# Performance work log

Measured on AMD Instinct MI355X. Metric: run time of the kernel, lower is better.

The kernel has to match this reference:

```python
import jax, jax.numpy as jnp
import numpy as np

NUM_HEADS = 16
DK = 64
DV = 64
MASK_FILL = -10000000000.0


def setup_inputs() -> dict:
    key = jax.random.key(0)
    kq, kk, kv, km = jax.random.split(key, 4)
    B, L, D = 2, 2048, NUM_HEADS * DK
    Q = jax.random.normal(kq, (B, L, D), dtype=jnp.float32)
    K = jax.random.normal(kk, (B, L, D), dtype=jnp.float32)
    V = jax.random.normal(kv, (B, L, NUM_HEADS * DV), dtype=jnp.float32)
    mask = jax.random.randint(km, (B, L, L), 0, 2).astype(jnp.bool_)
    return {"Q": Q, "K": K, "V": V, "mask": mask}


def reference(Q, K, V, mask):
    B, Lq, _ = Q.shape
    Lk = K.shape[1]
    # split heads: [B, H, L, d]
    q = Q.reshape(B, Lq, NUM_HEADS, DK).transpose(0, 2, 1, 3)
    k = K.reshape(B, Lk, NUM_HEADS, DK).transpose(0, 2, 1, 3)
    v = V.reshape(B, Lk, NUM_HEADS, DV).transpose(0, 2, 1, 3)
    # scores [B, H, Lq, Lk]; NOTE: original masks BEFORE scaling by 1/sqrt(dk)
    scores = jnp.einsum("bhqd,bhkd->bhqk", q, k)
    scores = jnp.where(mask[:, None, :, :], MASK_FILL, scores)
    scores = scores / jnp.sqrt(jnp.asarray(DK, dtype=scores.dtype))
    attn = jax.nn.softmax(scores, axis=-1)
    out = jnp.einsum("bhqk,bhkd->bhqd", attn, v)  # [B, H, Lq, dv]
    # concat heads back: [B, Lq, H*dv]
    return out.transpose(0, 2, 1, 3).reshape(B, Lq, NUM_HEADS * DV)
```

## Files before the change

kernel.cpp:

```cpp
#include <hip/hip_runtime.h>
#include <hip/hip_bf16.h>

#define NH 16
#define DH 64
#define LL 2048
#define DM 1024
#define SCALE2 0.1803368801111204f
#define GUARD_HI 60.0f
#define NT2 (LL / 128)

typedef __attribute__((ext_vector_type(4))) float f32x4;
typedef __attribute__((ext_vector_type(8))) short bf16x8;
typedef __attribute__((ext_vector_type(4))) short bf16x4;

__device__ __forceinline__ unsigned pk2(float lo, float hi) {
    __hip_bfloat162 h = __float22bfloat162_rn(make_float2(lo, hi));
    union { __hip_bfloat162 h; unsigned u; } c; c.h = h; return c.u;
}
__device__ __forceinline__ bf16x8 cvt8(float4 a, float4 b) {
    union { bf16x8 v; unsigned u[4]; } r;
    r.u[0] = pk2(a.x, a.y); r.u[1] = pk2(a.z, a.w);
    r.u[2] = pk2(b.x, b.y); r.u[3] = pk2(b.z, b.w);
    return r.v;
}
__device__ __forceinline__ float exp2_fast(float x) {
    float y;
    asm("v_exp_f32 %0, %1" : "=v"(y) : "v"(x));
    return y;
}
__device__ __forceinline__ float keepf(float p, unsigned nw, int idx) {
    int k = (int)(nw << (31 - idx)) >> 31;
    unsigned pu = __builtin_bit_cast(unsigned, p) & (unsigned)k;
    return __builtin_bit_cast(float, pu);
}

__global__ __launch_bounds__(256) void pack_mask2(const void* __restrict__ mask,
                                                  unsigned* __restrict__ bits)
{
    const int tid = threadIdx.x;
    const int lane = tid & 63;
    const int* mw = (const int*)mask;
    unsigned long long bad = __ballot((unsigned)mw[lane] > 1u);
    const bool is_int = (bad == 0ULL);

    const int wid = blockIdx.x * 256 + tid;
    const int g = wid & 3;
    const int t = (wid >> 2) & 15;
    const int q64 = wid >> 6;
    unsigned m = 0;
    if (is_int) {
        const int* p = (const int*)mask + (size_t)q64 * LL + t * 128 + 4 * g;
        #pragma unroll
        for (int sub = 0; sub < 2; ++sub)
            #pragma unroll
            for (int ki = 0; ki < 4; ++ki) {
                int4 v = *(const int4*)(p + sub * 64 + ki * 16);
                int base = sub * 16 + ki * 4;
                m |= (v.x ? 1u : 0u) << base;
                m |= (v.y ? 1u : 0u) << (base + 1);
                m |= (v.z ? 1u : 0u) << (base + 2);
                m |= (v.w ? 1u : 0u) << (base + 3);
            }
    } else {
        const unsigned char* pb = (const unsigned char*)mask
                                + (size_t)q64 * LL + t * 128 + 4 * g;
        #pragma unroll
        for (int sub = 0; sub < 2; ++sub)
            #pragma unroll
            for (int ki = 0; ki < 4; ++ki) {
                unsigned v = *(const unsigned*)(pb + sub * 64 + ki * 16);
                int base = sub * 16 + ki * 4;
                m |= (v & 1u) << base;
                m |= ((v >> 8) & 1u) << (base + 1);
                m |= ((v >> 16) & 1u) << (base + 2);
                m |= ((v >> 24) & 1u) << (base + 3);
            }
    }
    bits[wid] = ~m;
}

__global__ __launch_bounds__(256) void prep_k(const float* __restrict__ K,
                                              short* __restrict__ Kb)
{
    const int kt = blockIdx.x, h = blockIdx.y, b = blockIdx.z;
    const int tid = threadIdx.x;
    const int key = tid >> 2;
    const int c8 = (tid & 3) * 2;
    const float* src = K + ((size_t)b * LL + kt * 64 + key) * DM + h * DH + c8 * 8;
    float4 a = *(const float4*)(src);
    float4 bb = *(const float4*)(src + 4);
    float4 c = *(const float4*)(src + 8);
    float4 d = *(const float4*)(src + 12);
    short* dst = Kb + (((size_t)(b * NH + h) * 32 + kt) << 12);
    *(bf16x8*)&dst[key * 64 + ((c8 ^ (key & 7)) << 3)] = cvt8(a, bb);
    *(bf16x8*)&dst[key * 64 + (((c8 + 1) ^ (key & 7)) << 3)] = cvt8(c, d);
}

__global__ __launch_bounds__(256) void prep_v(const float* __restrict__ V,
                                              short* __restrict__ Vb)
{
    const int kt = blockIdx.x, h = blockIdx.y, b = blockIdx.z;
    const int tid = threadIdx.x;
    const int kp = tid & 31;
    const int dv8 = tid >> 5;
    const float* s0 = V + ((size_t)b * LL + kt * 64 + 2 * kp) * DM + h * DH + dv8 * 8;
    float4 a0 = *(const float4*)(s0);
    float4 a1 = *(const float4*)(s0 + 4);
    float4 b0 = *(const float4*)(s0 + DM);
    float4 b1 = *(const float4*)(s0 + DM + 4);
    float av[8] = {a0.x, a0.y, a0.z, a0.w, a1.x, a1.y, a1.z, a1.w};
    float bv[8] = {b0.x, b0.y, b0.z, b0.w, b1.x, b1.y, b1.z, b1.w};
    short* dst = Vb + (((size_t)(b * NH + h) * 32 + kt) << 12);
    const int grp = ((kp >> 4) << 2) | ((kp >> 1) & 3);
    const int sub4 = (((kp >> 3) & 1) << 2) | ((kp & 1) << 1);
    #pragma unroll
    for (int j = 0; j < 8; ++j) {
        int dv = dv8 * 8 + j;
        int off = dv * 64 + ((grp ^ (dv & 7)) << 3) + sub4;
        *(unsigned*)&dst[off] = pk2(av[j], bv[j]);
    }
}

__global__ __launch_bounds__(512, 4) void mha_fwd2(
    const float* __restrict__ Q, const short* __restrict__ Kb,
    const short* __restrict__ Vb, const unsigned* __restrict__ mbits,
    float* __restrict__ out)
{
    const int bid = blockIdx.x;
    const int xcd = bid & 7;
    const int j = bid >> 3;
    const int pair = xcd * 4 + (j >> 4);
    const int qblk = j & 15;
    const int h = pair & 15;
    const int b = pair >> 4;

    const int tid = threadIdx.x;
    const int w = tid >> 6;
    const int lane = tid & 63;
    const int lq = lane & 15;
    const int g = lane >> 4;

    const int qbase = qblk * 128 + w * 16;

    __shared__ short Kt[2][2][4096];
    __shared__ short Vt[2][2][4096];

    const short* Ktile0 = Kb + ((size_t)(b * NH + h) << 17);
    const short* Vtile0 = Vb + ((size_t)(b * NH + h) << 17);
    const unsigned* Mp = mbits + ((size_t)b * LL + qbase + lq) * 64 + g;

    unsigned mnext = Mp[0];
    #pragma unroll
    for (int sub = 0; sub < 2; ++sub) {
        __builtin_amdgcn_global_load_lds(
            (const unsigned*)(Ktile0 + sub * 4096 + w * 512 + lane * 8),
            (unsigned*)&Kt[0][sub][w * 512], 16, 0, 0);
        __builtin_amdgcn_global_load_lds(
            (const unsigned*)(Vtile0 + sub * 4096 + w * 512 + lane * 8),
            (unsigned*)&Vt[0][sub][w * 512], 16, 0, 0);
    }

    bf16x8 qf[2];
    {
        const float* qrow = Q + ((size_t)b * LL + qbase + lq) * DM + h * DH;
        #pragma unroll
        for (int half = 0; half < 2; ++half) {
            const float* src = qrow + half * 32 + g * 8;
            float4 a = *(const float4*)(src);
            float4 c = *(const float4*)(src + 4);
            a.x *= SCALE2; a.y *= SCALE2; a.z *= SCALE2; a.w *= SCALE2;
            c.x *= SCALE2; c.y *= SCALE2; c.z *= SCALE2; c.w *= SCALE2;
            qf[half] = cvt8(a, c);
        }
    }

    f32x4 o[4];
    #pragma unroll
    for (int t = 0; t < 4; ++t) o[t] = (f32x4){0.f, 0.f, 0.f, 0.f};
    f32x4 l_acc = (f32x4){0.f, 0.f, 0.f, 0.f};
    float m_shift = 0.f;
    const bf16x4 ones = {(short)0x3F80, (short)0x3F80, (short)0x3F80, (short)0x3F80};

    asm volatile("s_waitcnt vmcnt(0)" ::: "memory");
    __builtin_amdgcn_s_barrier();

    #pragma unroll 2
    for (int t = 0; t < NT2; ++t) {
        const int cur = t & 1;
        const unsigned nword = mnext;
        if (t + 1 < NT2) {
            mnext = Mp[(t + 1) * 4];
            const short* kb = Ktile0 + (size_t)(t + 1) * 8192;
            const short* vb = Vtile0 + (size_t)(t + 1) * 8192;
            #pragma unroll
            for (int sub = 0; sub < 2; ++sub) {
                __builtin_amdgcn_global_load_lds(
                    (const unsigned*)(kb + sub * 4096 + w * 512 + lane * 8),
                    (unsigned*)&Kt[cur ^ 1][sub][w * 512], 16, 0, 0);
                __builtin_amdgcn_global_load_lds(
                    (const unsigned*)(vb + sub * 4096 + w * 512 + lane * 8),
                    (unsigned*)&Vt[cur ^ 1][sub][w * 512], 16, 0, 0);
            }
            asm volatile("s_waitcnt vmcnt(5)" ::: "memory");
        } else {
            asm volatile("s_waitcnt vmcnt(0)" ::: "memory");
        }
        __builtin_amdgcn_s_barrier();
        __builtin_amdgcn_sched_barrier(0);

        f32x4 sAB[2][4];
        __builtin_amdgcn_s_setprio(1);
        #pragma unroll
        for (int sub = 0; sub < 2; ++sub)
            #pragma unroll
            for (int ki = 0; ki < 4; ++ki) {
                const int row = ki * 16 + lq;
                bf16x8 k0 = *(const bf16x8*)
                    &Kt[cur][sub][row * 64 + ((g ^ (lq & 7)) << 3)];
                bf16x8 k1 = *(const bf16x8*)
                    &Kt[cur][sub][row * 64 + (((4 + g) ^ (lq & 7)) << 3)];
                f32x4 acc = (f32x4){0.f, 0.f, 0.f, 0.f};
                acc = __builtin_amdgcn_mfma_f32_16x16x32_bf16(k0, qf[0], acc, 0, 0, 0);
                acc = __builtin_amdgcn_mfma_f32_16x16x32_bf16(k1, qf[1], acc, 0, 0, 0);
                sAB[sub][ki] = acc;
            }
        __builtin_amdgcn_s_setprio(0);

        float mm[8];
        #pragma unroll
        for (int i = 0; i < 8; ++i) {
            f32x4 v = sAB[i >> 2][i & 3];
            mm[i] = fmaxf(fmaxf(v[0], v[1]), fmaxf(v[2], v[3]));
        }
        float mx = fmaxf(fmaxf(fmaxf(mm[0], mm[1]), fmaxf(mm[2], mm[3])),
                         fmaxf(fmaxf(mm[4], mm[5]), fmaxf(mm[6], mm[7])));
        if (__builtin_expect(m_shift != 0.0f, 0)) {
            #pragma unroll
            for (int i = 0; i < 8; ++i) sAB[i >> 2][i & 3] = sAB[i >> 2][i & 3] - m_shift;
            mx -= m_shift;
        }
        if (!__all(mx <= GUARD_HI)) {
            float tmax = fmaxf(mx, __shfl_xor(mx, 16, 64));
            tmax = fmaxf(tmax, __shfl_xor(tmax, 32, 64));
            float shift = tmax - 30.0f;
            m_shift += shift;
            float alpha = exp2_fast(-shift);
            #pragma unroll
            for (int q = 0; q < 4; ++q) {
                o[q][0] *= alpha; o[q][1] *= alpha;
                o[q][2] *= alpha; o[q][3] *= alpha;
            }
            l_acc[0] *= alpha; l_acc[1] *= alpha;
            l_acc[2] *= alpha; l_acc[3] *= alpha;
            #pragma unroll
            for (int i = 0; i < 8; ++i) sAB[i >> 2][i & 3] = sAB[i >> 2][i & 3] - shift;
        }

        #pragma unroll
        for (int sub = 0; sub < 2; ++sub) {
            union { bf16x4 v; unsigned u[2]; } pf[4];
            #pragma unroll
            for (int ki = 0; ki < 4; ++ki) {
                f32x4 sv = sAB[sub][ki];
                const int base = sub * 16 + ki * 4;
                float p0 = keepf(exp2_fast(sv[0]), nword, base + 0);
                float p1 = keepf(exp2_fast(sv[1]), nword, base + 1);
                float p2 = keepf(exp2_fast(sv[2]), nword, base + 2);
                float p3 = keepf(exp2_fast(sv[3]), nword, base + 3);
                pf[ki].u[0] = pk2(p0, p1);
                pf[ki].u[1] = pk2(p2, p3);
                l_acc = __builtin_amdgcn_mfma_f32_16x16x16bf16_1k(ones, pf[ki].v, l_acc, 0, 0, 0);
            }
            __builtin_amdgcn_s_setprio(1);
            #pragma unroll
            for (int P = 0; P < 2; ++P)
                #pragma unroll
                for (int q = 0; q < 4; ++q) {
                    const int row = 16 * q + lq;
                    bf16x8 v8 = *(const bf16x8*)
                        &Vt[cur][sub][row * 64 + ((((P << 2) + g) ^ (lq & 7)) << 3)];
                    bf16x4 vlo = {v8[0], v8[1], v8[2], v8[3]};
                    bf16x4 vhi = {v8[4], v8[5], v8[6], v8[7]};
                    o[q] = __builtin_amdgcn_mfma_f32_16x16x16bf16_1k(vlo, pf[2 * P].v, o[q], 0, 0, 0);
                    o[q] = __builtin_amdgcn_mfma_f32_16x16x16bf16_1k(vhi, pf[2 * P + 1].v, o[q], 0, 0, 0);
                }
            __builtin_amdgcn_s_setprio(0);
        }

        __builtin_amdgcn_sched_barrier(0);
        __builtin_amdgcn_s_barrier();
    }

    float inv = __builtin_amdgcn_rcpf(l_acc[0]);
    float* orow = out + ((size_t)b * LL + qbase + lq) * DM + h * DH;
    #pragma unroll
    for (int t = 0; t < 4; ++t) {
        float4 ov;
        ov.x = o[t][0] * inv; ov.y = o[t][1] * inv;
        ov.z = o[t][2] * inv; ov.w = o[t][3] * inv;
        *(float4*)(orow + 16 * t + 4 * g) = ov;
    }
}

extern "C" void kernel_launch(void* const* d_in, const int* in_sizes, int n_in,
                              void* d_out, int out_size, void* d_ws, size_t ws_size,
                              hipStream_t stream) {
    const float* Q = (const float*)d_in[0];
    const float* K = (const float*)d_in[1];
    const float* V = (const float*)d_in[2];
    const void* mask = d_in[3];
    float* out = (float*)d_out;

    unsigned* bits = (unsigned*)d_ws;
    const size_t MASK_B = (size_t)2 * LL * 64 * 4;
    const size_t KV_B = (size_t)2 * NH * 32 * 4096 * 2;
    short* Kb = (short*)((char*)d_ws + MASK_B);
    short* Vb = (short*)((char*)d_ws + MASK_B + KV_B);

    pack_mask2<<<dim3(2 * LL * 64 / 256), dim3(256), 0, stream>>>(mask, bits);
    prep_k<<<dim3(32, NH, 2), dim3(256), 0, stream>>>(K, Kb);
    prep_v<<<dim3(32, NH, 2), dim3(256), 0, stream>>>(V, Vb);
    mha_fwd2<<<dim3(512), dim3(512), 0, stream>>>(Q, Kb, Vb, bits, out);
}
```

Baseline: 80.69 us.

## Switch attention kernel to 32x32x16 MFMA with 32-query waves

```diff
diff --git a/kernel.cpp b/kernel.cpp
--- a/kernel.cpp
+++ b/kernel.cpp
@@ -10,8 +10,8 @@
 #define NT2 (LL / 128)
 
 typedef __attribute__((ext_vector_type(4))) float f32x4;
+typedef __attribute__((ext_vector_type(16))) float f32x16;
 typedef __attribute__((ext_vector_type(8))) short bf16x8;
-typedef __attribute__((ext_vector_type(4))) short bf16x4;
 
 __device__ __forceinline__ unsigned pk2(float lo, float hi) {
     __hip_bfloat162 h = __float22bfloat162_rn(make_float2(lo, hi));
@@ -34,7 +34,7 @@
     return __builtin_bit_cast(float, pu);
 }
 
-__global__ __launch_bounds__(256) void pack_mask2(const void* __restrict__ mask,
+__global__ __launch_bounds__(256) void pack_mask4(const void* __restrict__ mask,
                                                   unsigned* __restrict__ bits)
 {
     const int tid = threadIdx.x;
@@ -44,18 +44,20 @@
     const bool is_int = (bad == 0ULL);
 
     const int wid = blockIdx.x * 256 + tid;
-    const int g = wid & 3;
-    const int t = (wid >> 2) & 15;
-    const int q64 = wid >> 6;
+    const int kb = wid & 3;
+    const int q = (wid >> 2) & 2047;
+    const int t = (wid >> 13) & 15;
+    const int b = wid >> 17;
     unsigned m = 0;
     if (is_int) {
-        const int* p = (const int*)mask + (size_t)q64 * LL + t * 128 + 4 * g;
-        #pragma unroll
-        for (int sub = 0; sub < 2; ++sub)
-            #pragma unroll
-            for (int ki = 0; ki < 4; ++ki) {
-                int4 v = *(const int4*)(p + sub * 64 + ki * 16);
-                int base = sub * 16 + ki * 4;
+        const int* p = (const int*)mask + ((size_t)b * 2048 + q) * 2048
+                     + t * 128 + kb * 32;
+        #pragma unroll
+        for (int h = 0; h < 2; ++h)
+            #pragma unroll
+            for (int blk = 0; blk < 4; ++blk) {
+                int4 v = *(const int4*)(p + 8 * blk + 4 * h);
+                int base = 8 * blk + 4 * h;
                 m |= (v.x ? 1u : 0u) << base;
                 m |= (v.y ? 1u : 0u) << (base + 1);
                 m |= (v.z ? 1u : 0u) << (base + 2);
@@ -63,13 +65,13 @@
             }
     } else {
         const unsigned char* pb = (const unsigned char*)mask
-                                + (size_t)q64 * LL + t * 128 + 4 * g;
-        #pragma unroll
-        for (int sub = 0; sub < 2; ++sub)
-            #pragma unroll
-            for (int ki = 0; ki < 4; ++ki) {
-                unsigned v = *(const unsigned*)(pb + sub * 64 + ki * 16);
-                int base = sub * 16 + ki * 4;
+                                + ((size_t)b * 2048 + q) * 2048 + t * 128 + kb * 32;
+        #pragma unroll
+        for (int h = 0; h < 2; ++h)
+            #pragma unroll
+            for (int blk = 0; blk < 4; ++blk) {
+                unsigned v = *(const unsigned*)(pb + 8 * blk + 4 * h);
+                int base = 8 * blk + 4 * h;
                 m |= (v & 1u) << base;
                 m |= ((v >> 8) & 1u) << (base + 1);
                 m |= ((v >> 16) & 1u) << (base + 2);
@@ -111,17 +113,20 @@
     float av[8] = {a0.x, a0.y, a0.z, a0.w, a1.x, a1.y, a1.z, a1.w};
     float bv[8] = {b0.x, b0.y, b0.z, b0.w, b1.x, b1.y, b1.z, b1.w};
     short* dst = Vb + (((size_t)(b * NH + h) * 32 + kt) << 12);
-    const int grp = ((kp >> 4) << 2) | ((kp >> 1) & 3);
-    const int sub4 = (((kp >> 3) & 1) << 2) | ((kp & 1) << 1);
+    const int w16 = (2 * kp) & 15;
+    const int kg = kp >> 3;
+    const int half = (w16 >> 2) & 1;
+    const int i0 = (w16 & 3) + 4 * (w16 >> 3);
+    const int sg = kg * 2 + half;
     #pragma unroll
     for (int j = 0; j < 8; ++j) {
         int dv = dv8 * 8 + j;
-        int off = dv * 64 + ((grp ^ (dv & 7)) << 3) + sub4;
+        int off = dv * 64 + ((sg ^ (dv & 7)) << 3) + i0;
         *(unsigned*)&dst[off] = pk2(av[j], bv[j]);
     }
 }
 
-__global__ __launch_bounds__(512, 4) void mha_fwd2(
+__global__ __launch_bounds__(256, 2) void mha_fwd3(
     const float* __restrict__ Q, const short* __restrict__ Kb,
     const short* __restrict__ Vb, const unsigned* __restrict__ mbits,
     float* __restrict__ out)
@@ -131,55 +136,56 @@
     const int j = bid >> 3;
     const int pair = xcd * 4 + (j >> 4);
     const int qblk = j & 15;
-    const int h = pair & 15;
+    const int hd = pair & 15;
     const int b = pair >> 4;
 
     const int tid = threadIdx.x;
     const int w = tid >> 6;
     const int lane = tid & 63;
-    const int lq = lane & 15;
-    const int g = lane >> 4;
-
-    const int qbase = qblk * 128 + w * 16;
+    const int lq = lane & 31;
+    const int hh = lane >> 5;
+
+    const int qbase = qblk * 128 + w * 32;
 
     __shared__ short Kt[2][2][4096];
     __shared__ short Vt[2][2][4096];
 
-    const short* Ktile0 = Kb + ((size_t)(b * NH + h) << 17);
-    const short* Vtile0 = Vb + ((size_t)(b * NH + h) << 17);
-    const unsigned* Mp = mbits + ((size_t)b * LL + qbase + lq) * 64 + g;
-
-    unsigned mnext = Mp[0];
+    const short* Ktile0 = Kb + ((size_t)(b * NH + hd) << 17);
+    const short* Vtile0 = Vb + ((size_t)(b * NH + hd) << 17);
+    const unsigned* Mp = mbits + (size_t)b * (16 * 8192) + (qbase + lq) * 4;
+
+    uint4 mreg = *(const uint4*)(Mp);
     #pragma unroll
-    for (int sub = 0; sub < 2; ++sub) {
-        __builtin_amdgcn_global_load_lds(
-            (const unsigned*)(Ktile0 + sub * 4096 + w * 512 + lane * 8),
-            (unsigned*)&Kt[0][sub][w * 512], 16, 0, 0);
-        __builtin_amdgcn_global_load_lds(
-            (const unsigned*)(Vtile0 + sub * 4096 + w * 512 + lane * 8),
-            (unsigned*)&Vt[0][sub][w * 512], 16, 0, 0);
-    }
-
-    bf16x8 qf[2];
+    for (int sub = 0; sub < 2; ++sub)
+        #pragma unroll
+        for (int i = 0; i < 2; ++i) {
+            __builtin_amdgcn_global_load_lds(
+                (const unsigned*)(Ktile0 + sub * 4096 + w * 1024 + i * 512 + lane * 8),
+                (unsigned*)&Kt[0][sub][w * 1024 + i * 512 + lane * 8], 16, 0, 0);
+            __builtin_amdgcn_global_load_lds(
+                (const unsigned*)(Vtile0 + sub * 4096 + w * 1024 + i * 512 + lane * 8),
+                (unsigned*)&Vt[0][sub][w * 1024 + i * 512 + lane * 8], 16, 0, 0);
+        }
+
+    bf16x8 qf[4];
     {
-        const float* qrow = Q + ((size_t)b * LL + qbase + lq) * DM + h * DH;
-        #pragma unroll
-        for (int half = 0; half < 2; ++half) {
-            const float* src = qrow + half * 32 + g * 8;
-            float4 a = *(const float4*)(src);
-            float4 c = *(const float4*)(src + 4);
+        const float* qp = Q + ((size_t)b * LL + qbase + lq) * DM + hd * DH + 8 * hh;
+        #pragma unroll
+        for (int d16 = 0; d16 < 4; ++d16) {
+            float4 a = *(const float4*)(qp + 16 * d16);
+            float4 c = *(const float4*)(qp + 16 * d16 + 4);
             a.x *= SCALE2; a.y *= SCALE2; a.z *= SCALE2; a.w *= SCALE2;
             c.x *= SCALE2; c.y *= SCALE2; c.z *= SCALE2; c.w *= SCALE2;
-            qf[half] = cvt8(a, c);
-        }
-    }
-
-    f32x4 o[4];
+            qf[d16] = cvt8(a, c);
+        }
+    }
+
+    f32x16 o0, o1;
     #pragma unroll
-    for (int t = 0; t < 4; ++t) o[t] = (f32x4){0.f, 0.f, 0.f, 0.f};
-    f32x4 l_acc = (f32x4){0.f, 0.f, 0.f, 0.f};
+    for (int i = 0; i < 16; ++i) { o0[i] = 0.f; o1[i] = 0.f; }
+    float l_own = 0.f;
     float m_shift = 0.f;
-    const bf16x4 ones = {(short)0x3F80, (short)0x3F80, (short)0x3F80, (short)0x3F80};
+    const int sh4 = 4 * hh;
 
     asm volatile("s_waitcnt vmcnt(0)" ::: "memory");
     __builtin_amdgcn_s_barrier();
@@ -187,118 +193,137 @@
     #pragma unroll 2
     for (int t = 0; t < NT2; ++t) {
         const int cur = t & 1;
-        const unsigned nword = mnext;
+        const uint4 m4 = mreg;
         if (t + 1 < NT2) {
-            mnext = Mp[(t + 1) * 4];
-            const short* kb = Ktile0 + (size_t)(t + 1) * 8192;
-            const short* vb = Vtile0 + (size_t)(t + 1) * 8192;
-            #pragma unroll
-            for (int sub = 0; sub < 2; ++sub) {
-                __builtin_amdgcn_global_load_lds(
-                    (const unsigned*)(kb + sub * 4096 + w * 512 + lane * 8),
-                    (unsigned*)&Kt[cur ^ 1][sub][w * 512], 16, 0, 0);
-                __builtin_amdgcn_global_load_lds(
-                    (const unsigned*)(vb + sub * 4096 + w * 512 + lane * 8),
-                    (unsigned*)&Vt[cur ^ 1][sub][w * 512], 16, 0, 0);
-            }
-            asm volatile("s_waitcnt vmcnt(5)" ::: "memory");
+            mreg = *(const uint4*)(Mp + (size_t)(t + 1) * 8192);
+            const short* kb_ = Ktile0 + (size_t)(t + 1) * 8192;
+            const short* vb_ = Vtile0 + (size_t)(t + 1) * 8192;
+            #pragma unroll
+            for (int sub = 0; sub < 2; ++sub)
+                #pragma unroll
+                for (int i = 0; i < 2; ++i) {
+                    __builtin_amdgcn_global_load_lds(
+                        (const unsigned*)(kb_ + sub * 4096 + w * 1024 + i * 512 + lane * 8),
+                        (unsigned*)&Kt[cur ^ 1][sub][w * 1024 + i * 512 + lane * 8], 16, 0, 0);
+                    __builtin_amdgcn_global_load_lds(
+                        (const unsigned*)(vb_ + sub * 4096 + w * 1024 + i * 512 + lane * 8),
+                        (unsigned*)&Vt[cur ^ 1][sub][w * 1024 + i * 512 + lane * 8], 16, 0, 0);
+                }
+            asm volatile("s_waitcnt vmcnt(9)" ::: "memory");
         } else {
             asm volatile("s_waitcnt vmcnt(0)" ::: "memory");
         }
         __builtin_amdgcn_s_barrier();
         __builtin_amdgcn_sched_barrier(0);
 
-        f32x4 sAB[2][4];
+        f32x16 s[4];
         __builtin_amdgcn_s_setprio(1);
         #pragma unroll
-        for (int sub = 0; sub < 2; ++sub)
-            #pragma unroll
-            for (int ki = 0; ki < 4; ++ki) {
-                const int row = ki * 16 + lq;
-                bf16x8 k0 = *(const bf16x8*)
-                    &Kt[cur][sub][row * 64 + ((g ^ (lq & 7)) << 3)];
-                bf16x8 k1 = *(const bf16x8*)
-                    &Kt[cur][sub][row * 64 + (((4 + g) ^ (lq & 7)) << 3)];
-                f32x4 acc = (f32x4){0.f, 0.f, 0.f, 0.f};
-                acc = __builtin_amdgcn_mfma_f32_16x16x32_bf16(k0, qf[0], acc, 0, 0, 0);
-                acc = __builtin_amdgcn_mfma_f32_16x16x32_bf16(k1, qf[1], acc, 0, 0, 0);
-                sAB[sub][ki] = acc;
+        for (int kb2 = 0; kb2 < 4; ++kb2) {
+            const int sub = kb2 >> 1;
+            const int keyrow = (kb2 & 1) * 32 + lq;
+            const int swz = keyrow & 7;
+            f32x16 acc;
+            #pragma unroll
+            for (int i = 0; i < 16; ++i) acc[i] = 0.f;
+            #pragma unroll
+            for (int d16 = 0; d16 < 4; ++d16) {
+                bf16x8 kf = *(const bf16x8*)
+                    &Kt[cur][sub][keyrow * 64 + (((2 * d16 + hh) ^ swz) << 3)];
+                acc = __builtin_amdgcn_mfma_f32_32x32x16_bf16(kf, qf[d16], acc, 0, 0, 0);
             }
+            s[kb2] = acc;
+        }
         __builtin_amdgcn_s_setprio(0);
 
-        float mm[8];
-        #pragma unroll
-        for (int i = 0; i < 8; ++i) {
-            f32x4 v = sAB[i >> 2][i & 3];
-            mm[i] = fmaxf(fmaxf(v[0], v[1]), fmaxf(v[2], v[3]));
-        }
-        float mx = fmaxf(fmaxf(fmaxf(mm[0], mm[1]), fmaxf(mm[2], mm[3])),
-                         fmaxf(fmaxf(mm[4], mm[5]), fmaxf(mm[6], mm[7])));
+        float mx = -1e30f;
+        #pragma unroll
+        for (int kb2 = 0; kb2 < 4; ++kb2) {
+            float a0 = fmaxf(fmaxf(s[kb2][0], s[kb2][1]), fmaxf(s[kb2][2], s[kb2][3]));
+            float a1 = fmaxf(fmaxf(s[kb2][4], s[kb2][5]), fmaxf(s[kb2][6], s[kb2][7]));
+            float a2 = fmaxf(fmaxf(s[kb2][8], s[kb2][9]), fmaxf(s[kb2][10], s[kb2][11]));
+            float a3 = fmaxf(fmaxf(s[kb2][12], s[kb2][13]), fmaxf(s[kb2][14], s[kb2][15]));
+            mx = fmaxf(mx, fmaxf(fmaxf(a0, a1), fmaxf(a2, a3)));
+        }
         if (__builtin_expect(m_shift != 0.0f, 0)) {
             #pragma unroll
-            for (int i = 0; i < 8; ++i) sAB[i >> 2][i & 3] = sAB[i >> 2][i & 3] - m_shift;
+            for (int kb2 = 0; kb2 < 4; ++kb2)
+                #pragma unroll
+                for (int r = 0; r < 16; ++r) s[kb2][r] -= m_shift;
             mx -= m_shift;
         }
         if (!__all(mx <= GUARD_HI)) {
-            float tmax = fmaxf(mx, __shfl_xor(mx, 16, 64));
-            tmax = fmaxf(tmax, __shfl_xor(tmax, 32, 64));
+            float tmax = fmaxf(mx, __shfl_xor(mx, 32, 64));
             float shift = tmax - 30.0f;
             m_shift += shift;
             float alpha = exp2_fast(-shift);
             #pragma unroll
-            for (int q = 0; q < 4; ++q) {
-                o[q][0] *= alpha; o[q][1] *= alpha;
-                o[q][2] *= alpha; o[q][3] *= alpha;
+            for (int i = 0; i < 16; ++i) { o0[i] *= alpha; o1[i] *= alpha; }
+            l_own *= alpha;
+            #pragma unroll
+            for (int kb2 = 0; kb2 < 4; ++kb2)
+                #pragma unroll
+                for (int r = 0; r < 16; ++r) s[kb2][r] -= shift;
+        }
+
+        unsigned nws0 = m4.x >> sh4, nws1 = m4.y >> sh4;
+        unsigned nws2 = m4.z >> sh4, nws3 = m4.w >> sh4;
+        unsigned nws[4] = {nws0, nws1, nws2, nws3};
+        bf16x8 pfr[4][2];
+        float lsum = 0.f;
+        #pragma unroll
+        for (int kb2 = 0; kb2 < 4; ++kb2) {
+            float p[16];
+            #pragma unroll
+            for (int r = 0; r < 16; ++r)
+                p[r] = keepf(exp2_fast(s[kb2][r]), nws[kb2], 8 * (r >> 2) + (r & 3));
+            float q1[8];
+            #pragma unroll
+            for (int i = 0; i < 8; ++i) q1[i] = p[2 * i] + p[2 * i + 1];
+            lsum += ((q1[0] + q1[1]) + (q1[2] + q1[3]))
+                  + ((q1[4] + q1[5]) + (q1[6] + q1[7]));
+            union { bf16x8 v; unsigned u[4]; } pa, pb;
+            pa.u[0] = pk2(p[0], p[1]);  pa.u[1] = pk2(p[2], p[3]);
+            pa.u[2] = pk2(p[4], p[5]);  pa.u[3] = pk2(p[6], p[7]);
+            pb.u[0] = pk2(p[8], p[9]);  pb.u[1] = pk2(p[10], p[11]);
+            pb.u[2] = pk2(p[12], p[13]); pb.u[3] = pk2(p[14], p[15]);
+            pfr[kb2][0] = pa.v;
+            pfr[kb2][1] = pb.v;
+        }
+        l_own += lsum;
+
+        __builtin_amdgcn_s_setprio(1);
+        #pragma unroll
+        for (int kb2 = 0; kb2 < 4; ++kb2) {
+            const int sub = kb2 >> 1;
+            #pragma unroll
+            for (int kkb = 0; kkb < 2; ++kkb) {
+                const int m = (kb2 & 1) * 2 + kkb;
+                const int slot = ((2 * m + hh) ^ (lq & 7)) << 3;
+                bf16x8 v0 = *(const bf16x8*)&Vt[cur][sub][lq * 64 + slot];
+                bf16x8 v1 = *(const bf16x8*)&Vt[cur][sub][(32 + lq) * 64 + slot];
+                o0 = __builtin_amdgcn_mfma_f32_32x32x16_bf16(v0, pfr[kb2][kkb], o0, 0, 0, 0);
+                o1 = __builtin_amdgcn_mfma_f32_32x32x16_bf16(v1, pfr[kb2][kkb], o1, 0, 0, 0);
             }
-            l_acc[0] *= alpha; l_acc[1] *= alpha;
-            l_acc[2] *= alpha; l_acc[3] *= alpha;
-            #pragma unroll
-            for (int i = 0; i < 8; ++i) sAB[i >> 2][i & 3] = sAB[i >> 2][i & 3] - shift;
-        }
-
-        #pragma unroll
-        for (int sub = 0; sub < 2; ++sub) {
-            union { bf16x4 v; unsigned u[2]; } pf[4];
-            #pragma unroll
-            for (int ki = 0; ki < 4; ++ki) {
-                f32x4 sv = sAB[sub][ki];
-                const int base = sub * 16 + ki * 4;
-                float p0 = keepf(exp2_fast(sv[0]), nword, base + 0);
-                float p1 = keepf(exp2_fast(sv[1]), nword, base + 1);
-                float p2 = keepf(exp2_fast(sv[2]), nword, base + 2);
-                float p3 = keepf(exp2_fast(sv[3]), nword, base + 3);
-                pf[ki].u[0] = pk2(p0, p1);
-                pf[ki].u[1] = pk2(p2, p3);
-                l_acc = __builtin_amdgcn_mfma_f32_16x16x16bf16_1k(ones, pf[ki].v, l_acc, 0, 0, 0);
-            }
-            __builtin_amdgcn_s_setprio(1);
-            #pragma unroll
-            for (int P = 0; P < 2; ++P)
-                #pragma unroll
-                for (int q = 0; q < 4; ++q) {
-                    const int row = 16 * q + lq;
-                    bf16x8 v8 = *(const bf16x8*)
-                        &Vt[cur][sub][row * 64 + ((((P << 2) + g) ^ (lq & 7)) << 3)];
-                    bf16x4 vlo = {v8[0], v8[1], v8[2], v8[3]};
-                    bf16x4 vhi = {v8[4], v8[5], v8[6], v8[7]};
-                    o[q] = __builtin_amdgcn_mfma_f32_16x16x16bf16_1k(vlo, pf[2 * P].v, o[q], 0, 0, 0);
-                    o[q] = __builtin_amdgcn_mfma_f32_16x16x16bf16_1k(vhi, pf[2 * P + 1].v, o[q], 0, 0, 0);
-                }
-            __builtin_amdgcn_s_setprio(0);
-        }
+        }
+        __builtin_amdgcn_s_setprio(0);
 
         __builtin_amdgcn_sched_barrier(0);
         __builtin_amdgcn_s_barrier();
     }
 
-    float inv = __builtin_amdgcn_rcpf(l_acc[0]);
-    float* orow = out + ((size_t)b * LL + qbase + lq) * DM + h * DH;
+    float l = l_own + __shfl_xor(l_own, 32, 64);
+    float inv = __builtin_amdgcn_rcpf(l);
+    float* fout = out + ((size_t)b * LL + qbase + lq) * DM + hd * DH + 4 * hh;
     #pragma unroll
-    for (int t = 0; t < 4; ++t) {
-        float4 ov;
-        ov.x = o[t][0] * inv; ov.y = o[t][1] * inv;
-        ov.z = o[t][2] * inv; ov.w = o[t][3] * inv;
-        *(float4*)(orow + 16 * t + 4 * g) = ov;
+    for (int rg = 0; rg < 4; ++rg) {
+        float4 v0, v1;
+        v0.x = o0[4 * rg + 0] * inv; v0.y = o0[4 * rg + 1] * inv;
+        v0.z = o0[4 * rg + 2] * inv; v0.w = o0[4 * rg + 3] * inv;
+        v1.x = o1[4 * rg + 0] * inv; v1.y = o1[4 * rg + 1] * inv;
+        v1.z = o1[4 * rg + 2] * inv; v1.w = o1[4 * rg + 3] * inv;
+        *(float4*)(fout + 8 * rg) = v0;
+        *(float4*)(fout + 32 + 8 * rg) = v1;
     }
 }
 
@@ -312,13 +337,13 @@
     float* out = (float*)d_out;
 
     unsigned* bits = (unsigned*)d_ws;
-    const size_t MASK_B = (size_t)2 * LL * 64 * 4;
+    const size_t MASK_B = (size_t)2 * 16 * 2048 * 4 * 4;
     const size_t KV_B = (size_t)2 * NH * 32 * 4096 * 2;
     short* Kb = (short*)((char*)d_ws + MASK_B);
     short* Vb = (short*)((char*)d_ws + MASK_B + KV_B);
 
-    pack_mask2<<<dim3(2 * LL * 64 / 256), dim3(256), 0, stream>>>(mask, bits);
+    pack_mask4<<<dim3(2 * 16 * 2048 * 4 / 256), dim3(256), 0, stream>>>(mask, bits);
     prep_k<<<dim3(32, NH, 2), dim3(256), 0, stream>>>(K, Kb);
     prep_v<<<dim3(32, NH, 2), dim3(256), 0, stream>>>(V, Vb);
-    mha_fwd2<<<dim3(512), dim3(512), 0, stream>>>(Q, Kb, Vb, bits, out);
-}
+    mha_fwd3<<<dim3(512), dim3(256), 0, stream>>>(Q, Kb, Vb, bits, out);
+}
```

Measured after the change: 82.60 us. 1.02x slower.
